# Kernel tuning notes

Hardware: AMD Instinct MI355X
Metric: run time of the kernel (lower is better)

The kernel has to match this reference:

```python
import jax, jax.numpy as jnp
import numpy as np

WS, OWS, NH = 16, 24, 2          # window size, overlap window size (=int(16*0.5)+16), num heads
PAD = (OWS - WS) // 2            # unfold padding = 4


def conv2d(x, w, b):
    kh, kw = w.shape[2], w.shape[3]
    out = jax.lax.conv_general_dilated(x, w, (1, 1), [(kh // 2, kh // 2), (kw // 2, kw // 2)],
                                       dimension_numbers=('NCHW', 'OIHW', 'NCHW'))
    return out + b[None, :, None, None]


def layer_norm(x, g, b, eps=1e-5):
    m = x.mean(-1, keepdims=True)
    v = ((x - m) ** 2).mean(-1, keepdims=True)
    return (x - m) * jax.lax.rsqrt(v + eps) * g + b


def stem(depth, cw1, cb1, cw2, cb2, cw3, cb3, cw4, cb4, in_g, in_b):
    # BasicConv(1->8,k3,relu) -> (8->16,k1,relu) -> (16->16,k3,relu) -> (16->32,k1) -> InstanceNorm2d(32,affine)
    y = jax.nn.relu(conv2d(depth, cw1, cb1))
    y = jax.nn.relu(conv2d(y, cw2, cb2))
    y = jax.nn.relu(conv2d(y, cw3, cb3))
    y = conv2d(y, cw4, cb4)
    m = y.mean((2, 3), keepdims=True)
    v = ((y - m) ** 2).mean((2, 3), keepdims=True)
    return (y - m) * jax.lax.rsqrt(v + 1e-5) * in_g[None, :, None, None] + in_b[None, :, None, None]


def ocab(xq, ykv, rpi, n1g, n1b, wq, bq, wkv, bkv, rpb, wp, bp, n2g, n2b, mw1, mb1, mw2, mb2):
    # Overlapping cross-attention block (HAT-style OCAB, cross variant: q from xq, kv from ykv).
    b, c, h, w = xq.shape
    x = xq.transpose(0, 2, 3, 1)   # b h w c
    y = ykv.transpose(0, 2, 3, 1)
    shortcut = x
    q = layer_norm(x, n1g, n1b) @ wq + bq          # b h w c
    kv = layer_norm(y, n1g, n1b) @ wkv + bkv       # b h w 2c
    nhw, nww = h // WS, w // WS
    # non-overlapping query windows: (b*nw, WS*WS, c)
    qw = q.reshape(b, nhw, WS, nww, WS, c).transpose(0, 1, 3, 2, 4, 5).reshape(b * nhw * nww, WS * WS, c)
    # overlapping kv windows via unfold (patch channel order = (channel, kh, kw), same as torch unfold)
    patches = jax.lax.conv_general_dilated_patches(kv.transpose(0, 3, 1, 2), (OWS, OWS), (WS, WS),
                                                   [(PAD, PAD), (PAD, PAD)])  # b, 2c*OWS*OWS, nhw, nww
    patches = patches.reshape(b, 2, c, OWS * OWS, nhw * nww).transpose(1, 0, 4, 3, 2).reshape(2, b * nhw * nww, OWS * OWS, c)
    k, v = patches[0], patches[1]
    d = c // NH
    qh = qw.reshape(-1, WS * WS, NH, d).transpose(0, 2, 1, 3) * (d ** -0.5)
    kh = k.reshape(-1, OWS * OWS, NH, d).transpose(0, 2, 1, 3)
    vh = v.reshape(-1, OWS * OWS, NH, d).transpose(0, 2, 1, 3)
    attn = jnp.einsum('whqd,whkd->whqk', qh, kh)
    attn = attn + rpb[rpi].transpose(2, 0, 1)[None]  # rel-pos bias -> [1, NH, WS*WS, OWS*OWS]
    attn = jax.nn.softmax(attn, axis=-1)
    out = jnp.einsum('whqk,whkd->whqd', attn, vh).transpose(0, 2, 1, 3).reshape(-1, WS * WS, c)
    # window reverse
    out = out.reshape(b, nhw, nww, WS, WS, c).transpose(0, 1, 3, 2, 4, 5).reshape(b, h, w, c)
    out = out @ wp + bp + shortcut
    out = out + (jax.nn.gelu(layer_norm(out, n2g, n2b) @ mw1 + mb1) @ mw2 + mb2)  # mlp_ratio=2
    return out.transpose(0, 3, 1, 2)


def setup_inputs():
    key = jax.random.key(0)
    ks = jax.random.split(key, 16)
    B, C, H, W = 1, 32, 256, 256
    s = 0.05
    return dict(
        x=jax.random.normal(ks[0], (B, C, H, W), jnp.float32),
        depth=jax.random.normal(ks[1], (B, 1, H, W), jnp.float32),
        rpi=jax.random.randint(ks[2], (WS * WS, OWS * OWS), 0, (WS + OWS - 1) ** 2),
        cw1=jax.random.normal(ks[3], (8, 1, 3, 3)) * s, cb1=jnp.zeros(8),
        cw2=jax.random.normal(ks[4], (16, 8, 1, 1)) * s, cb2=jnp.zeros(16),
        cw3=jax.random.normal(ks[5], (16, 16, 3, 3)) * s, cb3=jnp.zeros(16),
        cw4=jax.random.normal(ks[6], (32, 16, 1, 1)) * s, cb4=jnp.zeros(32),
        in_g=jnp.ones(32), in_b=jnp.zeros(32),
        n1g=jnp.ones(C), n1b=jnp.zeros(C),
        wq=jax.random.normal(ks[7], (C, C)) * s, bq=jnp.zeros(C),
        wkv=jax.random.normal(ks[8], (C, 2 * C)) * s, bkv=jnp.zeros(2 * C),
        rpb=jax.random.normal(ks[9], ((WS + OWS - 1) ** 2, NH)) * 0.02,
        wp=jax.random.normal(ks[10], (C, C)) * s, bp=jnp.zeros(C),
        n2g=jnp.ones(C), n2b=jnp.zeros(C),
        mw1=jax.random.normal(ks[11], (C, 2 * C)) * s, mb1=jnp.zeros(2 * C),
        mw2=jax.random.normal(ks[12], (2 * C, C)) * s, mb2=jnp.zeros(C),
    )


def reference(x, depth, rpi, cw1, cb1, cw2, cb2, cw3, cb3, cw4, cb4, in_g, in_b,
              n1g, n1b, wq, bq, wkv, bkv, rpb, wp, bp, n2g, n2b, mw1, mb1, mw2, mb2):
    f = stem(depth, cw1, cb1, cw2, cb2, cw3, cb3, cw4, cb4, in_g, in_b)
    a = (n1g, n1b, wq, bq, wkv, bkv, rpb, wp, bp, n2g, n2b, mw1, mb1, mw2, mb2)
    out1 = ocab(x, f, rpi, *a)   # shared OCAB weights, called twice with swapped roles
    out2 = ocab(f, x, rpi, *a)
    return out1 + out2 + x
```

## Files before the change

kernel.cpp:

```cpp
#include <hip/hip_runtime.h>
#include <hip/hip_bf16.h>

#define HW 65536
#define KPAD 584

typedef __attribute__((ext_vector_type(8))) short bf8;
typedef __attribute__((ext_vector_type(4))) float f4;

__device__ __forceinline__ unsigned short f2b(float x) {
  unsigned int u = __float_as_uint(x);
  unsigned int r = (u + 0x7fff + ((u >> 16) & 1)) >> 16;
  return (unsigned short)r;
}
__device__ __forceinline__ unsigned int pk2(float lo, float hi) {
  return (__float_as_uint(hi) & 0xffff0000u) | (__float_as_uint(lo) >> 16);
}
__device__ __forceinline__ unsigned int pkrne(float lo, float hi) {
  return ((unsigned int)f2b(hi) << 16) | (unsigned int)f2b(lo);
}
__device__ __forceinline__ float blo(unsigned int u) { return __uint_as_float(u << 16); }
__device__ __forceinline__ float bhi(unsigned int u) { return __uint_as_float(u & 0xffff0000u); }
__device__ __forceinline__ float ex2(float x) { return __builtin_amdgcn_exp2f(x); }

__device__ __forceinline__ void stem_front_body(
    int bx, int t, const float* __restrict__ depth,
    const float* __restrict__ cw1, const float* __restrict__ cb1,
    const float* __restrict__ cw2, const float* __restrict__ cb2,
    float* __restrict__ t2) {
  int p = bx * 256 + t;
  int y = p >> 8, x = p & 255;
  float in9[9];
#pragma unroll
  for (int ky = 0; ky < 3; ky++)
#pragma unroll
    for (int kx = 0; kx < 3; kx++) {
      int yy = y + ky - 1, xx = x + kx - 1;
      bool ok = ((unsigned)yy < 256u) && ((unsigned)xx < 256u);
      in9[ky*3+kx] = ok ? depth[yy*256+xx] : 0.f;
    }
  float t1[8];
#pragma unroll
  for (int o = 0; o < 8; o++) {
    float s = cb1[o];
#pragma unroll
    for (int i = 0; i < 9; i++) s += in9[i] * cw1[o*9+i];
    t1[o] = fmaxf(s, 0.f);
  }
#pragma unroll
  for (int o = 0; o < 16; o++) {
    float s = cb2[o];
#pragma unroll
    for (int ci = 0; ci < 8; ci++) s += t1[ci] * cw2[o*8+ci];
    t2[o*HW + p] = fmaxf(s, 0.f);
  }
}

__device__ __forceinline__ void bias_body(
    int bx, int t, const int* __restrict__ rpi,
    const float* __restrict__ rpb, float* __restrict__ biasT) {
  int idx = bx*256 + t;
  int hd = idx / 147456;
  int rem = idx - hd*147456;
  int qt = rem / 9216;
  int r2 = rem - qt*9216;
  int kb = r2 >> 6;
  int q16 = (r2 >> 2) & 15;
  int r = r2 & 3;
  int key = kb*4 + r;
  int qq = qt*16 + q16;
  biasT[idx] = (rpb[rpi[qq*576 + key]*2 + hd] - 8.0f) * 1.44269504f;
}

__device__ __forceinline__ void lnmm48_body(
    int role, int bx, int t,
    unsigned int* ws16, float* gs, float* bs, float* b2s, float* as_, float* bbs_,
    const float* __restrict__ x, const float* __restrict__ t4,
    const float* __restrict__ part,
    const float* __restrict__ ig, const float* __restrict__ ib,
    const float* __restrict__ n1g, const float* __restrict__ n1b,
    const float* __restrict__ wq, const float* __restrict__ bq,
    const float* __restrict__ wkv, const float* __restrict__ bkv,
    unsigned int* __restrict__ q1, unsigned int* __restrict__ kv1,
    unsigned int* __restrict__ q2, unsigned int* __restrict__ kv2) {
  const float QS = 0.360673503f;
  bool ain = role >= 2;
  int slice = role & 1;
  const float* src = ain ? t4 : x;
  unsigned int* dq  = ain ? q2 : q1;
  unsigned int* dkv = ain ? kv1 : kv2;
  for (int i = t; i < 768; i += 256) {
    int c = i / 24, jw = i - c*24;
    int j = jw*2;
    float a, b;
    if (slice) { a = wkv[c*64 + 16 + j]; b = wkv[c*64 + 16 + j + 1]; }
    else if (j < 32) { a = wq[c*32 + j]; b = wq[c*32 + j + 1]; }
    else { a = wkv[c*64 + (j - 32)]; b = wkv[c*64 + (j - 31)]; }
    ws16[i] = pkrne(a, b);
  }
  if (t < 48) b2s[t] = slice ? bkv[16 + t] : (t < 32 ? bq[t] : bkv[t - 32]);
  if (t < 32) {
    gs[t] = n1g[t]; bs[t] = n1b[t];
    if (ain) {
      float s = 0.f, ss = 0.f;
#pragma unroll
      for (int k = 0; k < 16; k++) { s += part[t*16+k]; ss += part[512 + t*16+k]; }
      float m = s * (1.f/65536.f);
      float var = ss * (1.f/65536.f) - m*m;
      float a = rsqrtf(var + 1e-5f) * ig[t];
      as_[t] = a; bbs_[t] = ib[t] - m*a;
    }
  }
  __syncthreads();
  int p = bx*256 + t;
  float v[32]; float s = 0.f;
  if (ain) {
#pragma unroll
    for (int c = 0; c < 32; c++) { v[c] = src[c*HW+p]*as_[c] + bbs_[c]; s += v[c]; }
  } else {
#pragma unroll
    for (int c = 0; c < 32; c++) { v[c] = src[c*HW+p]; s += v[c]; }
  }
  float m = s * 0.03125f;
  float ss = 0.f;
#pragma unroll
  for (int c = 0; c < 32; c++) { float d = v[c]-m; ss += d*d; }
  float rs = rsqrtf(ss*0.03125f + 1e-5f);
  float acc[48];
#pragma unroll
  for (int j = 0; j < 48; j++) acc[j] = b2s[j];
#pragma unroll
  for (int c = 0; c < 32; c++) {
    float ln = (v[c]-m)*rs*gs[c] + bs[c];
    const uint4* w4 = (const uint4*)&ws16[c*24];
#pragma unroll
    for (int q4 = 0; q4 < 6; q4++) {
      uint4 w = w4[q4];
      acc[q4*8+0] += ln*blo(w.x); acc[q4*8+1] += ln*bhi(w.x);
      acc[q4*8+2] += ln*blo(w.y); acc[q4*8+3] += ln*bhi(w.y);
      acc[q4*8+4] += ln*blo(w.z); acc[q4*8+5] += ln*bhi(w.z);
      acc[q4*8+6] += ln*blo(w.w); acc[q4*8+7] += ln*bhi(w.w);
    }
  }
  if (slice == 0) {
#pragma unroll
    for (int j2 = 0; j2 < 16; j2++)
      dq[j2*HW+p] = pkrne(acc[2*j2]*QS, acc[2*j2+1]*QS);
#pragma unroll
    for (int c2 = 0; c2 < 8; c2++)
      dkv[c2*HW+p] = pkrne(acc[32+2*c2], acc[32+2*c2+1]);
  } else {
#pragma unroll
    for (int c2 = 0; c2 < 24; c2++)
      dkv[(8+c2)*HW+p] = pkrne(acc[2*c2], acc[2*c2+1]);
  }
}

__global__ __launch_bounds__(256) void k_misc(
    const float* __restrict__ depth,
    const float* __restrict__ cw1, const float* __restrict__ cb1,
    const float* __restrict__ cw2, const float* __restrict__ cb2,
    float* __restrict__ t2,
    const int* __restrict__ rpi, const float* __restrict__ rpb, float* __restrict__ biasT,
    const float* __restrict__ x, const float* __restrict__ t4,
    const float* __restrict__ part,
    const float* __restrict__ ig, const float* __restrict__ ib,
    const float* __restrict__ n1g, const float* __restrict__ n1b,
    const float* __restrict__ wq, const float* __restrict__ bq,
    const float* __restrict__ wkv, const float* __restrict__ bkv,
    unsigned int* q1, unsigned int* kv1, unsigned int* q2, unsigned int* kv2) {
  __shared__ __align__(16) unsigned int ws16[768];
  __shared__ float gs[32], bs[32], b2s[48], as_[32], bbs_[32];
  int id = blockIdx.x, t = threadIdx.x;
  if (id < 256) { stem_front_body(id, t, depth, cw1, cb1, cw2, cb2, t2); return; }
  if (id < 1408) { bias_body(id - 256, t, rpi, rpb, biasT); return; }
  int r = id - 1408;
  lnmm48_body(r >> 8, r & 255, t, ws16, gs, bs, b2s, as_, bbs_,
              x, t4, part, ig, ib, n1g, n1b, wq, bq, wkv, bkv, q1, kv1, q2, kv2);
}

__global__ __launch_bounds__(256) void k_lnmmB(
    const float* __restrict__ x, const float* __restrict__ t4,
    const float* __restrict__ part,
    const float* __restrict__ ig, const float* __restrict__ ib,
    const float* __restrict__ n1g, const float* __restrict__ n1b,
    const float* __restrict__ wq, const float* __restrict__ bq,
    const float* __restrict__ wkv, const float* __restrict__ bkv,
    unsigned int* q1, unsigned int* kv1, unsigned int* q2, unsigned int* kv2) {
  __shared__ __align__(16) unsigned int ws16[768];
  __shared__ float gs[32], bs[32], b2s[48], as_[32], bbs_[32];
  lnmm48_body(2 + blockIdx.y, blockIdx.x, threadIdx.x, ws16, gs, bs, b2s, as_, bbs_,
              x, t4, part, ig, ib, n1g, n1b, wq, bq, wkv, bkv, q1, kv1, q2, kv2);
}

__global__ __launch_bounds__(256) void k_conv3(
    const float* __restrict__ t2, const float* __restrict__ cw3,
    const float* __restrict__ cb3, float* __restrict__ t3) {
  int t = threadIdx.x;
  int p = blockIdx.x*256 + t;
  int og = blockIdx.y;
  int y = p >> 8, x = p & 255;
  float acc[4];
#pragma unroll
  for (int o = 0; o < 4; o++) acc[o] = cb3[og*4+o];
#pragma unroll 1
  for (int tap = 0; tap < 9; tap++) {
    int ky = tap/3 - 1, kx = tap - (tap/3)*3 - 1;
    int yy = y+ky, xx = x+kx;
    bool ok = ((unsigned)yy < 256u) && ((unsigned)xx < 256u);
    int pp = yy*256+xx;
#pragma unroll
    for (int ci = 0; ci < 16; ci++) {
      float v = ok ? t2[ci*HW+pp] : 0.f;
#pragma unroll
      for (int o = 0; o < 4; o++)
        acc[o] += v * cw3[(og*4+o)*144 + ci*9 + tap];
    }
  }
#pragma unroll
  for (int o = 0; o < 4; o++) t3[(og*4+o)*HW+p] = fmaxf(acc[o], 0.f);
}

__global__ __launch_bounds__(256) void k_conv4(
    const float* __restrict__ t3, const float* __restrict__ cw4,
    const float* __restrict__ cb4, float* __restrict__ t4) {
  int t = threadIdx.x;
  int p = blockIdx.x*256 + t;
  int og = blockIdx.y;
  float v[16];
#pragma unroll
  for (int ci = 0; ci < 16; ci++) v[ci] = t3[ci*HW+p];
#pragma unroll
  for (int o = 0; o < 8; o++) {
    int oo = og*8 + o;
    float s = cb4[oo];
#pragma unroll
    for (int ci = 0; ci < 16; ci++) s += v[ci]*cw4[oo*16+ci];
    t4[oo*HW+p] = s;
  }
}

__global__ __launch_bounds__(256) void k_instats1(const float* __restrict__ t4,
                                                  float* __restrict__ part) {
  int c = blockIdx.x >> 4, seg = blockIdx.x & 15;
  const float4* src = (const float4*)(t4 + c*HW + seg*4096);
  float s = 0.f, ss = 0.f;
  for (int i = threadIdx.x; i < 1024; i += 256) {
    float4 v = src[i];
    s  += v.x + v.y + v.z + v.w;
    ss += v.x*v.x + v.y*v.y + v.z*v.z + v.w*v.w;
  }
#pragma unroll
  for (int off = 32; off > 0; off >>= 1) {
    s  += __shfl_down(s, off, 64);
    ss += __shfl_down(ss, off, 64);
  }
  __shared__ float sh[8];
  int wid = threadIdx.x >> 6;
  if ((threadIdx.x & 63) == 0) { sh[wid] = s; sh[4+wid] = ss; }
  __syncthreads();
  if (threadIdx.x == 0) {
    part[blockIdx.x]       = sh[0]+sh[1]+sh[2]+sh[3];
    part[512 + blockIdx.x] = sh[4]+sh[5]+sh[6]+sh[7];
  }
}

__global__ __launch_bounds__(256, 4) void k_attn(
    const unsigned int* __restrict__ qA, const unsigned int* __restrict__ kvA,
    float* __restrict__ aoA,
    const unsigned int* __restrict__ qB, const unsigned int* __restrict__ kvB,
    float* __restrict__ aoB,
    const float* __restrict__ biasT) {
  __shared__ __align__(16) unsigned short Ks[576*16];
  __shared__ __align__(16) unsigned short Vt[16*KPAD];

  const unsigned int* q  = blockIdx.y ? qB  : qA;
  const unsigned int* kv = blockIdx.y ? kvB : kvA;
  float* ao              = blockIdx.y ? aoB : aoA;

  int id = blockIdx.x;
  int lin = ((id & 7) << 6) | (id >> 3);
  int wi = lin >> 1, hd = lin & 1;
  int wy = wi >> 4, wx = wi & 15;
  int t = threadIdx.x;
  int by = wy*16 - 4, bx = wx*16 - 4;
  int krow = hd*8, vrow = 16 + hd*8;

  int wave = t >> 6, lane = t & 63;
  int quad = lane >> 4, l16 = lane & 15;
  const bf8 zero8 = {0,0,0,0,0,0,0,0};

  bf8 qf[4];
#pragma unroll
  for (int qi = 0; qi < 4; qi++) {
    if (quad < 2) {
      int qt = wave*4 + qi;
      int prow = (wy*16 + qt)*256 + wx*16 + l16;
      union { unsigned int u[4]; bf8 v; } Q;
#pragma unroll
      for (int jw = 0; jw < 4; jw++)
        Q.u[jw] = q[(krow + quad*4 + jw)*HW + prow];
      qf[qi] = Q.v;
    } else {
      qf[qi] = zero8;
    }
  }

  for (int e = t; e < 576; e += 256) {
    int dy = e / 24, dx = e - dy*24;
    int yy = by + dy, xx = bx + dx;
    bool ok = ((unsigned)yy < 256u) && ((unsigned)xx < 256u);
    int pp = yy*256 + xx;
    int off = e & 31;
    int ppos = ((off & 12) << 1) + ((off >> 4) << 2) + (off & 3);
    int vcol = (e & ~31) + ppos;
    unsigned int kwd[8];
#pragma unroll
    for (int i = 0; i < 8; i++) kwd[i] = ok ? kv[(krow + i)*HW + pp] : 0u;
    *(uint4*)&Ks[e*16]     = *(const uint4*)&kwd[0];
    *(uint4*)&Ks[e*16 + 8] = *(const uint4*)&kwd[4];
#pragma unroll
    for (int i = 0; i < 8; i++) {
      unsigned int vw = ok ? kv[(vrow + i)*HW + pp] : 0u;
      Vt[(2*i)*KPAD + vcol]   = (unsigned short)vw;
      Vt[(2*i+1)*KPAD + vcol] = (unsigned short)(vw >> 16);
    }
  }
  __syncthreads();

  f4 oacc[4];
  float lr[4];
  const float* bb[4];
#pragma unroll
  for (int qi = 0; qi < 4; qi++) {
    int qt = wave*4 + qi;
    oacc[qi] = (f4){0.f,0.f,0.f,0.f};
    lr[qi] = 0.f;
    bb[qi] = biasT + (hd*16 + qt)*9216 + quad*64 + l16*4;
  }

#pragma unroll 2
  for (int kt2 = 0; kt2 < 18; kt2++) {
    int k0 = kt2 * 32;
    bf8 kf0 = zero8, kf1 = zero8;
    if (quad < 2) {
      kf0 = *(const bf8*)&Ks[(k0 + l16)*16 + quad*8];
      kf1 = *(const bf8*)&Ks[(k0 + 16 + l16)*16 + quad*8];
    }
    bf8 vf = *(const bf8*)&Vt[l16*KPAD + k0 + quad*8];
    __builtin_amdgcn_s_setprio(1);
#pragma unroll
    for (int qi = 0; qi < 4; qi++) {
      f4 b0 = *(const f4*)&bb[qi][k0*16];
      f4 b1 = *(const f4*)&bb[qi][(k0+16)*16];
      f4 s0 = __builtin_amdgcn_mfma_f32_16x16x32_bf16(kf0, qf[qi], b0, 0, 0, 0);
      f4 s1 = __builtin_amdgcn_mfma_f32_16x16x32_bf16(kf1, qf[qi], b1, 0, 0, 0);
      float p0[4], p1[4];
#pragma unroll
      for (int r = 0; r < 4; r++) {
        p0[r] = ex2(s0[r]);
        p1[r] = ex2(s1[r]);
        lr[qi] += p0[r] + p1[r];
      }
      union { unsigned int u[4]; bf8 v; } P;
      P.u[0] = pk2(p0[0], p0[1]); P.u[1] = pk2(p0[2], p0[3]);
      P.u[2] = pk2(p1[0], p1[1]); P.u[3] = pk2(p1[2], p1[3]);
      oacc[qi] = __builtin_amdgcn_mfma_f32_16x16x32_bf16(P.v, vf, oacc[qi], 0, 0, 0);
    }
    __builtin_amdgcn_s_setprio(0);
  }
#pragma unroll
  for (int qi = 0; qi < 4; qi++) {
    lr[qi] += __shfl_xor(lr[qi], 16, 64);
    lr[qi] += __shfl_xor(lr[qi], 32, 64);
  }
#pragma unroll
  for (int qi = 0; qi < 4; qi++) {
    int qt = wave*4 + qi;
#pragma unroll
    for (int r = 0; r < 4; r++) {
      float lv = __shfl(lr[qi], quad*4 + r, 64);
      int qw = qt*16 + quad*4 + r;
      ao[(hd*16 + l16)*HW + (wy*16 + (qw >> 4))*256 + wx*16 + (qw & 15)] = oacc[qi][r] / lv;
    }
  }
}

__global__ __launch_bounds__(256) void k_projmlp(
    const float* __restrict__ ao1, const float* __restrict__ ao2,
    const float* __restrict__ x, const float* __restrict__ t4,
    const float* __restrict__ part,
    const float* __restrict__ ig, const float* __restrict__ ib,
    const float* __restrict__ wp, const float* __restrict__ bp,
    const float* __restrict__ n2g, const float* __restrict__ n2b,
    const float* __restrict__ mw1, const float* __restrict__ mb1,
    const float* __restrict__ mw2, const float* __restrict__ mb2,
    float* __restrict__ out) {
  __shared__ __align__(16) float wps[1024];
  __shared__ __align__(16) float w1s[2048];
  __shared__ __align__(16) float w2s[2048];
  __shared__ float bps[32], b1s[64], b2s[32], gs[32], bs[32], as_[32], bbs_[32];
  int t = threadIdx.x;
  for (int i = t; i < 1024; i += 256) wps[i] = wp[i];
  for (int i = t; i < 2048; i += 256) { w1s[i] = mw1[i]; w2s[i] = mw2[i]; }
  if (t < 64) b1s[t] = mb1[t];
  if (t < 32) {
    bps[t] = bp[t]; b2s[t] = mb2[t]; gs[t] = n2g[t]; bs[t] = n2b[t];
    float s = 0.f, ss = 0.f;
#pragma unroll
    for (int k = 0; k < 16; k++) { s += part[t*16+k]; ss += part[512 + t*16+k]; }
    float m = s * (1.f/65536.f);
    float var = ss * (1.f/65536.f) - m*m;
    float a = rsqrtf(var + 1e-5f) * ig[t];
    as_[t] = a; bbs_[t] = ib[t] - m*a;
  }
  __syncthreads();
  int p  = blockIdx.x*128 + (t >> 1);
  int sg = t & 1;
  int jb = sg*16;

  float A[16], B[16];
#pragma unroll
  for (int jj = 0; jj < 16; jj++) { A[jj] = bps[jb+jj]; B[jj] = A[jj]; }
#pragma unroll
  for (int c = 0; c < 32; c++) {
    float va = ao1[c*HW+p];
    float vb = ao2[c*HW+p];
    const float4* w4 = (const float4*)&wps[c*32 + jb];
#pragma unroll
    for (int j4 = 0; j4 < 4; j4++) {
      float4 w = w4[j4];
      A[j4*4+0] += va*w.x; A[j4*4+1] += va*w.y; A[j4*4+2] += va*w.z; A[j4*4+3] += va*w.w;
      B[j4*4+0] += vb*w.x; B[j4*4+1] += vb*w.y; B[j4*4+2] += vb*w.z; B[j4*4+3] += vb*w.w;
    }
  }
  float OUT[16];
#pragma unroll
  for (int jj = 0; jj < 16; jj++) {
    float xv = x[(jb+jj)*HW+p];
    float tv = t4[(jb+jj)*HW+p]*as_[jb+jj] + bbs_[jb+jj];
    A[jj] += xv; B[jj] += tv;
    OUT[jj] = A[jj] + B[jj] + xv + 2.f*b2s[jb+jj];
  }
  float sA = 0.f, sB = 0.f;
#pragma unroll
  for (int jj = 0; jj < 16; jj++) { sA += A[jj]; sB += B[jj]; }
  sA += __shfl_xor(sA, 1, 64);
  sB += __shfl_xor(sB, 1, 64);
  float mA = sA * 0.03125f, mB = sB * 0.03125f;
  float ssA = 0.f, ssB = 0.f;
#pragma unroll
  for (int jj = 0; jj < 16; jj++) {
    float dA = A[jj]-mA, dB = B[jj]-mB;
    ssA += dA*dA; ssB += dB*dB;
  }
  ssA += __shfl_xor(ssA, 1, 64);
  ssB += __shfl_xor(ssB, 1, 64);
  float rsA = rsqrtf(ssA*0.03125f + 1e-5f);
  float rsB = rsqrtf(ssB*0.03125f + 1e-5f);
  float lnA_lo[16], lnA_hi[16], lnB_lo[16], lnB_hi[16];
#pragma unroll
  for (int jj = 0; jj < 16; jj++) {
    float ownA = (A[jj]-mA)*rsA*gs[jb+jj] + bs[jb+jj];
    float ownB = (B[jj]-mB)*rsB*gs[jb+jj] + bs[jb+jj];
    float othA = __shfl_xor(ownA, 1, 64);
    float othB = __shfl_xor(ownB, 1, 64);
    lnA_lo[jj] = sg ? othA : ownA;
    lnA_hi[jj] = sg ? ownA : othA;
    lnB_lo[jj] = sg ? othB : ownB;
    lnB_hi[jj] = sg ? ownB : othB;
  }
  float h0[32], h1[32];
#pragma unroll
  for (int kk = 0; kk < 32; kk++) { h0[kk] = b1s[sg*32+kk]; h1[kk] = h0[kk]; }
#pragma unroll
  for (int c = 0; c < 32; c++) {
    float l0 = (c < 16) ? lnA_lo[c] : lnA_hi[c-16];
    float l1 = (c < 16) ? lnB_lo[c] : lnB_hi[c-16];
    const float4* w4 = (const float4*)&w1s[c*64 + sg*32];
#pragma unroll
    for (int k4 = 0; k4 < 8; k4++) {
      float4 w = w4[k4];
      h0[k4*4+0] += l0*w.x; h0[k4*4+1] += l0*w.y; h0[k4*4+2] += l0*w.z; h0[k4*4+3] += l0*w.w;
      h1[k4*4+0] += l1*w.x; h1[k4*4+1] += l1*w.y; h1[k4*4+2] += l1*w.z; h1[k4*4+3] += l1*w.w;
    }
  }
#pragma unroll
  for (int kk = 0; kk < 32; kk++) {
    float x0 = h0[kk], x1 = h1[kk];
    float u0 = 0.7978845608f * (x0 + 0.044715f*x0*x0*x0);
    float u1 = 0.7978845608f * (x1 + 0.044715f*x1*x1*x1);
    float th0 = 1.f - 2.f/(1.f + __expf(2.f*u0));
    float th1 = 1.f - 2.f/(1.f + __expf(2.f*u1));
    h0[kk] = 0.5f*x0*(1.f + th0) + 0.5f*x1*(1.f + th1);
  }
  float plo[16], phi[16];
#pragma unroll
  for (int jj = 0; jj < 16; jj++) { plo[jj] = 0.f; phi[jj] = 0.f; }
#pragma unroll
  for (int kk = 0; kk < 32; kk++) {
    float gk = h0[kk];
    const float4* w4 = (const float4*)&w2s[(sg*32+kk)*32];
#pragma unroll
    for (int j4 = 0; j4 < 4; j4++) {
      float4 w = w4[j4];
      plo[j4*4+0] += gk*w.x; plo[j4*4+1] += gk*w.y;
      plo[j4*4+2] += gk*w.z; plo[j4*4+3] += gk*w.w;
    }
#pragma unroll
    for (int j4 = 0; j4 < 4; j4++) {
      float4 w = w4[4+j4];
      phi[j4*4+0] += gk*w.x; phi[j4*4+1] += gk*w.y;
      phi[j4*4+2] += gk*w.z; phi[j4*4+3] += gk*w.w;
    }
  }
#pragma unroll
  for (int jj = 0; jj < 16; jj++) {
    float send = sg ? plo[jj] : phi[jj];
    float recv = __shfl_xor(send, 1, 64);
    float own  = sg ? phi[jj] : plo[jj];
    out[(jb+jj)*HW + p] = OUT[jj] + own + recv;
  }
}

extern "C" void kernel_launch(void* const* d_in, const int* in_sizes, int n_in,
                              void* d_out, int out_size, void* d_ws, size_t ws_size,
                              hipStream_t stream) {
  const float* x    = (const float*)d_in[0];
  const float* depth= (const float*)d_in[1];
  const int*   rpi  = (const int*)d_in[2];
  const float* cw1  = (const float*)d_in[3],  *cb1 = (const float*)d_in[4];
  const float* cw2  = (const float*)d_in[5],  *cb2 = (const float*)d_in[6];
  const float* cw3  = (const float*)d_in[7],  *cb3 = (const float*)d_in[8];
  const float* cw4  = (const float*)d_in[9],  *cb4 = (const float*)d_in[10];
  const float* in_g = (const float*)d_in[11], *in_b = (const float*)d_in[12];
  const float* n1g  = (const float*)d_in[13], *n1b = (const float*)d_in[14];
  const float* wq   = (const float*)d_in[15], *bq  = (const float*)d_in[16];
  const float* wkv  = (const float*)d_in[17], *bkv = (const float*)d_in[18];
  const float* rpb  = (const float*)d_in[19];
  const float* wp   = (const float*)d_in[20], *bp  = (const float*)d_in[21];
  const float* n2g  = (const float*)d_in[22], *n2b = (const float*)d_in[23];
  const float* mw1  = (const float*)d_in[24], *mb1 = (const float*)d_in[25];
  const float* mw2  = (const float*)d_in[26], *mb2 = (const float*)d_in[27];

  float* W   = (float*)d_ws;
  float* o1  = (float*)d_out;

  float* t4    = W;
  unsigned int* q1  = (unsigned int*)(W + 2097152);
  unsigned int* q2  = (unsigned int*)(W + 3145728);
  unsigned int* kv1 = (unsigned int*)(W + 4194304);
  unsigned int* kv2 = (unsigned int*)(W + 6291456);
  float* ao1   = W + 8388608;
  float* ao2   = W + 10485760;
  float* biasT = W + 12582912;
  float* part  = W + 12877824;
  float* t2 = ao1;
  float* t3 = ao2;

  k_misc   <<<1920, 256, 0, stream>>>(depth, cw1, cb1, cw2, cb2, t2,
                                      rpi, rpb, biasT,
                                      x, t4, part, in_g, in_b, n1g, n1b,
                                      wq, bq, wkv, bkv, q1, kv1, q2, kv2);
  k_conv3  <<<dim3(256,4), 256, 0, stream>>>(t2, cw3, cb3, t3);
  k_conv4  <<<dim3(256,4), 256, 0, stream>>>(t3, cw4, cb4, t4);
  k_instats1<<<512, 256, 0, stream>>>(t4, part);
  k_lnmmB  <<<dim3(256,2), 256, 0, stream>>>(x, t4, part, in_g, in_b, n1g, n1b,
                                             wq, bq, wkv, bkv, q1, kv1, q2, kv2);
  k_attn   <<<dim3(512,2), 256, 0, stream>>>(q1, kv1, ao1, q2, kv2, ao2, biasT);
  k_projmlp<<<512, 256, 0, stream>>>(ao1, ao2, x, t4, part, in_g, in_b,
                                     wp, bp, n2g, n2b, mw1, mb1, mw2, mb2, o1);
}
```

Measured before the change: 238.9 us.

## Pack attention bias as bf16 pairs, fuse instance stats into conv4, MFMA row sums

Stores the relative position bias as packed bf16 pairs instead of fp32, which halves bias memory traffic in the attention loop and shrinks the bias-building part of k_misc. Instance-norm statistics are now reduced inside k_conv4 with wave shuffles and atomics, removing the separate k_instats1 launch and its reread of t4. Softmax row sums are computed with an extra MFMA against a ones vector instead of scalar adds and cross-lane shuffles. The risks are reduced bias precision, the constant -8 offset being dropped from the bias, and single-pass float atomics for the variance, which can lose precision.

```diff
diff --git a/kernel.cpp b/kernel.cpp
--- a/kernel.cpp
+++ b/kernel.cpp
@@ -55,20 +55,22 @@
   }
 }
 
-__device__ __forceinline__ void bias_body(
+__device__ __forceinline__ void bias_pk_body(
     int bx, int t, const int* __restrict__ rpi,
-    const float* __restrict__ rpb, float* __restrict__ biasT) {
+    const float* __restrict__ rpb, unsigned int* __restrict__ biasPk) {
   int idx = bx*256 + t;
-  int hd = idx / 147456;
-  int rem = idx - hd*147456;
-  int qt = rem / 9216;
-  int r2 = rem - qt*9216;
-  int kb = r2 >> 6;
-  int q16 = (r2 >> 2) & 15;
-  int r = r2 & 3;
-  int key = kb*4 + r;
-  int qq = qt*16 + q16;
-  biasT[idx] = (rpb[rpi[qq*576 + key]*2 + hd] - 8.0f) * 1.44269504f;
+  int hd = idx / 36864;
+  int rem = idx - hd*36864;
+  int qt = rem / 4608;
+  int r2 = rem - qt*4608;
+  int kt2 = r2 >> 8;
+  int w8 = r2 & 255;
+  int quad = w8 >> 6, q = (w8 >> 2) & 15, r = w8 & 3;
+  int klo = kt2*32 + quad*4 + r;
+  int qq = qt*16 + q;
+  float lo = rpb[rpi[qq*576 + klo]*2 + hd] * 1.44269504f;
+  float hi = rpb[rpi[qq*576 + klo + 16]*2 + hd] * 1.44269504f;
+  biasPk[idx] = pkrne(lo, hi);
 }
 
 __device__ __forceinline__ void lnmm48_body(
@@ -101,11 +103,8 @@
   if (t < 32) {
     gs[t] = n1g[t]; bs[t] = n1b[t];
     if (ain) {
-      float s = 0.f, ss = 0.f;
-#pragma unroll
-      for (int k = 0; k < 16; k++) { s += part[t*16+k]; ss += part[512 + t*16+k]; }
-      float m = s * (1.f/65536.f);
-      float var = ss * (1.f/65536.f) - m*m;
+      float m = part[t] * (1.f/65536.f);
+      float var = part[32+t] * (1.f/65536.f) - m*m;
       float a = rsqrtf(var + 1e-5f) * ig[t];
       as_[t] = a; bbs_[t] = ib[t] - m*a;
     }
@@ -160,9 +159,9 @@
     const float* __restrict__ cw1, const float* __restrict__ cb1,
     const float* __restrict__ cw2, const float* __restrict__ cb2,
     float* __restrict__ t2,
-    const int* __restrict__ rpi, const float* __restrict__ rpb, float* __restrict__ biasT,
+    const int* __restrict__ rpi, const float* __restrict__ rpb,
+    unsigned int* __restrict__ biasPk, float* __restrict__ part,
     const float* __restrict__ x, const float* __restrict__ t4,
-    const float* __restrict__ part,
     const float* __restrict__ ig, const float* __restrict__ ib,
     const float* __restrict__ n1g, const float* __restrict__ n1b,
     const float* __restrict__ wq, const float* __restrict__ bq,
@@ -172,8 +171,12 @@
   __shared__ float gs[32], bs[32], b2s[48], as_[32], bbs_[32];
   int id = blockIdx.x, t = threadIdx.x;
   if (id < 256) { stem_front_body(id, t, depth, cw1, cb1, cw2, cb2, t2); return; }
-  if (id < 1408) { bias_body(id - 256, t, rpi, rpb, biasT); return; }
-  int r = id - 1408;
+  if (id < 544) {
+    if (id == 256 && t < 64) part[t] = 0.f;
+    bias_pk_body(id - 256, t, rpi, rpb, biasPk);
+    return;
+  }
+  int r = id - 544;
   lnmm48_body(r >> 8, r & 255, t, ws16, gs, bs, b2s, as_, bbs_,
               x, t4, part, ig, ib, n1g, n1b, wq, bq, wkv, bkv, q1, kv1, q2, kv2);
 }
@@ -222,13 +225,15 @@
 
 __global__ __launch_bounds__(256) void k_conv4(
     const float* __restrict__ t3, const float* __restrict__ cw4,
-    const float* __restrict__ cb4, float* __restrict__ t4) {
+    const float* __restrict__ cb4, float* __restrict__ t4,
+    float* __restrict__ part) {
   int t = threadIdx.x;
   int p = blockIdx.x*256 + t;
   int og = blockIdx.y;
   float v[16];
 #pragma unroll
   for (int ci = 0; ci < 16; ci++) v[ci] = t3[ci*HW+p];
+  float s8[8], q8[8];
 #pragma unroll
   for (int o = 0; o < 8; o++) {
     int oo = og*8 + o;
@@ -236,31 +241,27 @@
 #pragma unroll
     for (int ci = 0; ci < 16; ci++) s += v[ci]*cw4[oo*16+ci];
     t4[oo*HW+p] = s;
-  }
-}
-
-__global__ __launch_bounds__(256) void k_instats1(const float* __restrict__ t4,
-                                                  float* __restrict__ part) {
-  int c = blockIdx.x >> 4, seg = blockIdx.x & 15;
-  const float4* src = (const float4*)(t4 + c*HW + seg*4096);
-  float s = 0.f, ss = 0.f;
-  for (int i = threadIdx.x; i < 1024; i += 256) {
-    float4 v = src[i];
-    s  += v.x + v.y + v.z + v.w;
-    ss += v.x*v.x + v.y*v.y + v.z*v.z + v.w*v.w;
-  }
-#pragma unroll
-  for (int off = 32; off > 0; off >>= 1) {
-    s  += __shfl_down(s, off, 64);
-    ss += __shfl_down(ss, off, 64);
-  }
-  __shared__ float sh[8];
-  int wid = threadIdx.x >> 6;
-  if ((threadIdx.x & 63) == 0) { sh[wid] = s; sh[4+wid] = ss; }
+    s8[o] = s; q8[o] = s*s;
+  }
+#pragma unroll
+  for (int off = 1; off < 64; off <<= 1) {
+#pragma unroll
+    for (int o = 0; o < 8; o++) {
+      s8[o] += __shfl_xor(s8[o], off, 64);
+      q8[o] += __shfl_xor(q8[o], off, 64);
+    }
+  }
+  __shared__ float red[4][16];
+  int wid = t >> 6, lane = t & 63;
+  if (lane == 0) {
+#pragma unroll
+    for (int o = 0; o < 8; o++) { red[wid][o] = s8[o]; red[wid][8+o] = q8[o]; }
+  }
   __syncthreads();
-  if (threadIdx.x == 0) {
-    part[blockIdx.x]       = sh[0]+sh[1]+sh[2]+sh[3];
-    part[512 + blockIdx.x] = sh[4]+sh[5]+sh[6]+sh[7];
+  if (t < 16) {
+    float acc = red[0][t] + red[1][t] + red[2][t] + red[3][t];
+    int o = t & 7;
+    atomicAdd(&part[(t < 8 ? 0 : 32) + og*8 + o], acc);
   }
 }
 
@@ -269,7 +270,7 @@
     float* __restrict__ aoA,
     const unsigned int* __restrict__ qB, const unsigned int* __restrict__ kvB,
     float* __restrict__ aoB,
-    const float* __restrict__ biasT) {
+    const unsigned int* __restrict__ biasPk) {
   __shared__ __align__(16) unsigned short Ks[576*16];
   __shared__ __align__(16) unsigned short Vt[16*KPAD];
 
@@ -288,6 +289,7 @@
   int wave = t >> 6, lane = t & 63;
   int quad = lane >> 4, l16 = lane & 15;
   const bf8 zero8 = {0,0,0,0,0,0,0,0};
+  const bf8 ones8 = {0x3F80,0x3F80,0x3F80,0x3F80,0x3F80,0x3F80,0x3F80,0x3F80};
 
   bf8 qf[4];
 #pragma unroll
@@ -328,15 +330,13 @@
   __syncthreads();
 
   f4 oacc[4];
-  float lr[4];
-  const float* bb[4];
+  f4 lacc[4];
 #pragma unroll
   for (int qi = 0; qi < 4; qi++) {
-    int qt = wave*4 + qi;
     oacc[qi] = (f4){0.f,0.f,0.f,0.f};
-    lr[qi] = 0.f;
-    bb[qi] = biasT + (hd*16 + qt)*9216 + quad*64 + l16*4;
-  }
+    lacc[qi] = (f4){0.f,0.f,0.f,0.f};
+  }
+  unsigned int bb0 = (unsigned)((hd*8 + wave*4)*4608 + quad*64 + l16*4);
 
 #pragma unroll 2
   for (int kt2 = 0; kt2 < 18; kt2++) {
@@ -350,8 +350,12 @@
     __builtin_amdgcn_s_setprio(1);
 #pragma unroll
     for (int qi = 0; qi < 4; qi++) {
-      f4 b0 = *(const f4*)&bb[qi][k0*16];
-      f4 b1 = *(const f4*)&bb[qi][(k0+16)*16];
+      uint4 bw = *(const uint4*)&biasPk[bb0 + qi*4608 + kt2*256];
+      f4 b0, b1;
+      b0[0] = blo(bw.x); b1[0] = bhi(bw.x);
+      b0[1] = blo(bw.y); b1[1] = bhi(bw.y);
+      b0[2] = blo(bw.z); b1[2] = bhi(bw.z);
+      b0[3] = blo(bw.w); b1[3] = bhi(bw.w);
       f4 s0 = __builtin_amdgcn_mfma_f32_16x16x32_bf16(kf0, qf[qi], b0, 0, 0, 0);
       f4 s1 = __builtin_amdgcn_mfma_f32_16x16x32_bf16(kf1, qf[qi], b1, 0, 0, 0);
       float p0[4], p1[4];
@@ -359,28 +363,23 @@
       for (int r = 0; r < 4; r++) {
         p0[r] = ex2(s0[r]);
         p1[r] = ex2(s1[r]);
-        lr[qi] += p0[r] + p1[r];
       }
       union { unsigned int u[4]; bf8 v; } P;
       P.u[0] = pk2(p0[0], p0[1]); P.u[1] = pk2(p0[2], p0[3]);
       P.u[2] = pk2(p1[0], p1[1]); P.u[3] = pk2(p1[2], p1[3]);
       oacc[qi] = __builtin_amdgcn_mfma_f32_16x16x32_bf16(P.v, vf, oacc[qi], 0, 0, 0);
+      lacc[qi] = __builtin_amdgcn_mfma_f32_16x16x32_bf16(P.v, ones8, lacc[qi], 0, 0, 0);
     }
     __builtin_amdgcn_s_setprio(0);
-  }
-#pragma unroll
-  for (int qi = 0; qi < 4; qi++) {
-    lr[qi] += __shfl_xor(lr[qi], 16, 64);
-    lr[qi] += __shfl_xor(lr[qi], 32, 64);
   }
 #pragma unroll
   for (int qi = 0; qi < 4; qi++) {
     int qt = wave*4 + qi;
 #pragma unroll
     for (int r = 0; r < 4; r++) {
-      float lv = __shfl(lr[qi], quad*4 + r, 64);
       int qw = qt*16 + quad*4 + r;
-      ao[(hd*16 + l16)*HW + (wy*16 + (qw >> 4))*256 + wx*16 + (qw & 15)] = oacc[qi][r] / lv;
+      ao[(hd*16 + l16)*HW + (wy*16 + (qw >> 4))*256 + wx*16 + (qw & 15)] =
+          oacc[qi][r] / lacc[qi][r];
     }
   }
 }
@@ -405,11 +404,8 @@
   if (t < 64) b1s[t] = mb1[t];
   if (t < 32) {
     bps[t] = bp[t]; b2s[t] = mb2[t]; gs[t] = n2g[t]; bs[t] = n2b[t];
-    float s = 0.f, ss = 0.f;
-#pragma unroll
-    for (int k = 0; k < 16; k++) { s += part[t*16+k]; ss += part[512 + t*16+k]; }
-    float m = s * (1.f/65536.f);
-    float var = ss * (1.f/65536.f) - m*m;
+    float m = part[t] * (1.f/65536.f);
+    float var = part[32+t] * (1.f/65536.f) - m*m;
     float a = rsqrtf(var + 1e-5f) * ig[t];
     as_[t] = a; bbs_[t] = ib[t] - m*a;
   }
@@ -552,21 +548,20 @@
   unsigned int* kv2 = (unsigned int*)(W + 6291456);
   float* ao1   = W + 8388608;
   float* ao2   = W + 10485760;
-  float* biasT = W + 12582912;
+  unsigned int* biasPk = (unsigned int*)(W + 12582912);
   float* part  = W + 12877824;
   float* t2 = ao1;
   float* t3 = ao2;
 
-  k_misc   <<<1920, 256, 0, stream>>>(depth, cw1, cb1, cw2, cb2, t2,
-                                      rpi, rpb, biasT,
-                                      x, t4, part, in_g, in_b, n1g, n1b,
+  k_misc   <<<1056, 256, 0, stream>>>(depth, cw1, cb1, cw2, cb2, t2,
+                                      rpi, rpb, biasPk, part,
+                                      x, t4, in_g, in_b, n1g, n1b,
                                       wq, bq, wkv, bkv, q1, kv1, q2, kv2);
   k_conv3  <<<dim3(256,4), 256, 0, stream>>>(t2, cw3, cb3, t3);
-  k_conv4  <<<dim3(256,4), 256, 0, stream>>>(t3, cw4, cb4, t4);
-  k_instats1<<<512, 256, 0, stream>>>(t4, part);
+  k_conv4  <<<dim3(256,4), 256, 0, stream>>>(t3, cw4, cb4, t4, part);
   k_lnmmB  <<<dim3(256,2), 256, 0, stream>>>(x, t4, part, in_g, in_b, n1g, n1b,
                                              wq, bq, wkv, bkv, q1, kv1, q2, kv2);
-  k_attn   <<<dim3(512,2), 256, 0, stream>>>(q1, kv1, ao1, q2, kv2, ao2, biasT);
+  k_attn   <<<dim3(512,2), 256, 0, stream>>>(q1, kv1, ao1, q2, kv2, ao2, biasPk);
   k_projmlp<<<512, 256, 0, stream>>>(ao1, ao2, x, t4, part, in_g, in_b,
                                      wp, bp, n2g, n2b, mw1, mb1, mw2, mb2, o1);
 }
```

Result: slower. 349.0 us (+46.1%).

## Pack attention bias to bf16 pairs and compute row sums via MFMA

Applied to the files above, without the earlier changes.

The relative-position bias table is stored as packed bf16 pairs, with the two key halves in one word. This halves the bias bytes the attention kernel reads per tile and shrinks the bias-generation launch. The softmax denominator is now accumulated by an extra MFMA of the probability tile against a ones matrix, replacing per-lane scalar sums and the cross-lane shuffles. The constant -8 offset on the bias is dropped and bias precision drops to bf16, which risks exp2 overflow or accuracy differences.

```diff
diff --git a/kernel.cpp b/kernel.cpp
--- a/kernel.cpp
+++ b/kernel.cpp
@@ -55,20 +55,22 @@
   }
 }
 
-__device__ __forceinline__ void bias_body(
+__device__ __forceinline__ void bias_pk_body(
     int bx, int t, const int* __restrict__ rpi,
-    const float* __restrict__ rpb, float* __restrict__ biasT) {
+    const float* __restrict__ rpb, unsigned int* __restrict__ biasPk) {
   int idx = bx*256 + t;
-  int hd = idx / 147456;
-  int rem = idx - hd*147456;
-  int qt = rem / 9216;
-  int r2 = rem - qt*9216;
-  int kb = r2 >> 6;
-  int q16 = (r2 >> 2) & 15;
-  int r = r2 & 3;
-  int key = kb*4 + r;
+  int hd = idx / 73728;
+  int rem = idx - hd*73728;
+  int qt = rem / 4608;
+  int r2 = rem - qt*4608;
+  int kt2 = r2 >> 8;
+  int w8 = r2 & 255;
+  int quad = w8 >> 6, q16 = (w8 >> 2) & 15, r = w8 & 3;
+  int klo = kt2*32 + quad*4 + r;
   int qq = qt*16 + q16;
-  biasT[idx] = (rpb[rpi[qq*576 + key]*2 + hd] - 8.0f) * 1.44269504f;
+  float lo = rpb[rpi[qq*576 + klo]*2 + hd] * 1.44269504f;
+  float hi = rpb[rpi[qq*576 + klo + 16]*2 + hd] * 1.44269504f;
+  biasPk[idx] = pkrne(lo, hi);
 }
 
 __device__ __forceinline__ void lnmm48_body(
@@ -160,7 +162,8 @@
     const float* __restrict__ cw1, const float* __restrict__ cb1,
     const float* __restrict__ cw2, const float* __restrict__ cb2,
     float* __restrict__ t2,
-    const int* __restrict__ rpi, const float* __restrict__ rpb, float* __restrict__ biasT,
+    const int* __restrict__ rpi, const float* __restrict__ rpb,
+    unsigned int* __restrict__ biasPk,
     const float* __restrict__ x, const float* __restrict__ t4,
     const float* __restrict__ part,
     const float* __restrict__ ig, const float* __restrict__ ib,
@@ -172,8 +175,8 @@
   __shared__ float gs[32], bs[32], b2s[48], as_[32], bbs_[32];
   int id = blockIdx.x, t = threadIdx.x;
   if (id < 256) { stem_front_body(id, t, depth, cw1, cb1, cw2, cb2, t2); return; }
-  if (id < 1408) { bias_body(id - 256, t, rpi, rpb, biasT); return; }
-  int r = id - 1408;
+  if (id < 832) { bias_pk_body(id - 256, t, rpi, rpb, biasPk); return; }
+  int r = id - 832;
   lnmm48_body(r >> 8, r & 255, t, ws16, gs, bs, b2s, as_, bbs_,
               x, t4, part, ig, ib, n1g, n1b, wq, bq, wkv, bkv, q1, kv1, q2, kv2);
 }
@@ -269,7 +272,7 @@
     float* __restrict__ aoA,
     const unsigned int* __restrict__ qB, const unsigned int* __restrict__ kvB,
     float* __restrict__ aoB,
-    const float* __restrict__ biasT) {
+    const unsigned int* __restrict__ biasPk) {
   __shared__ __align__(16) unsigned short Ks[576*16];
   __shared__ __align__(16) unsigned short Vt[16*KPAD];
 
@@ -288,6 +291,7 @@
   int wave = t >> 6, lane = t & 63;
   int quad = lane >> 4, l16 = lane & 15;
   const bf8 zero8 = {0,0,0,0,0,0,0,0};
+  const bf8 ones8 = {0x3F80,0x3F80,0x3F80,0x3F80,0x3F80,0x3F80,0x3F80,0x3F80};
 
   bf8 qf[4];
 #pragma unroll
@@ -328,15 +332,13 @@
   __syncthreads();
 
   f4 oacc[4];
-  float lr[4];
-  const float* bb[4];
+  f4 lacc[4];
 #pragma unroll
   for (int qi = 0; qi < 4; qi++) {
-    int qt = wave*4 + qi;
     oacc[qi] = (f4){0.f,0.f,0.f,0.f};
-    lr[qi] = 0.f;
-    bb[qi] = biasT + (hd*16 + qt)*9216 + quad*64 + l16*4;
-  }
+    lacc[qi] = (f4){0.f,0.f,0.f,0.f};
+  }
+  unsigned int bb0 = (unsigned)((hd*16 + wave*4)*4608 + quad*64 + l16*4);
 
 #pragma unroll 2
   for (int kt2 = 0; kt2 < 18; kt2++) {
@@ -350,8 +352,12 @@
     __builtin_amdgcn_s_setprio(1);
 #pragma unroll
     for (int qi = 0; qi < 4; qi++) {
-      f4 b0 = *(const f4*)&bb[qi][k0*16];
-      f4 b1 = *(const f4*)&bb[qi][(k0+16)*16];
+      uint4 bw = *(const uint4*)&biasPk[bb0 + qi*4608 + kt2*256];
+      f4 b0, b1;
+      b0[0] = blo(bw.x); b1[0] = bhi(bw.x);
+      b0[1] = blo(bw.y); b1[1] = bhi(bw.y);
+      b0[2] = blo(bw.z); b1[2] = bhi(bw.z);
+      b0[3] = blo(bw.w); b1[3] = bhi(bw.w);
       f4 s0 = __builtin_amdgcn_mfma_f32_16x16x32_bf16(kf0, qf[qi], b0, 0, 0, 0);
       f4 s1 = __builtin_amdgcn_mfma_f32_16x16x32_bf16(kf1, qf[qi], b1, 0, 0, 0);
       float p0[4], p1[4];
@@ -359,28 +365,23 @@
       for (int r = 0; r < 4; r++) {
         p0[r] = ex2(s0[r]);
         p1[r] = ex2(s1[r]);
-        lr[qi] += p0[r] + p1[r];
       }
       union { unsigned int u[4]; bf8 v; } P;
       P.u[0] = pk2(p0[0], p0[1]); P.u[1] = pk2(p0[2], p0[3]);
       P.u[2] = pk2(p1[0], p1[1]); P.u[3] = pk2(p1[2], p1[3]);
       oacc[qi] = __builtin_amdgcn_mfma_f32_16x16x32_bf16(P.v, vf, oacc[qi], 0, 0, 0);
+      lacc[qi] = __builtin_amdgcn_mfma_f32_16x16x32_bf16(P.v, ones8, lacc[qi], 0, 0, 0);
     }
     __builtin_amdgcn_s_setprio(0);
-  }
-#pragma unroll
-  for (int qi = 0; qi < 4; qi++) {
-    lr[qi] += __shfl_xor(lr[qi], 16, 64);
-    lr[qi] += __shfl_xor(lr[qi], 32, 64);
   }
 #pragma unroll
   for (int qi = 0; qi < 4; qi++) {
     int qt = wave*4 + qi;
 #pragma unroll
     for (int r = 0; r < 4; r++) {
-      float lv = __shfl(lr[qi], quad*4 + r, 64);
       int qw = qt*16 + quad*4 + r;
-      ao[(hd*16 + l16)*HW + (wy*16 + (qw >> 4))*256 + wx*16 + (qw & 15)] = oacc[qi][r] / lv;
+      ao[(hd*16 + l16)*HW + (wy*16 + (qw >> 4))*256 + wx*16 + (qw & 15)] =
+          oacc[qi][r] / lacc[qi][r];
     }
   }
 }
@@ -552,13 +553,13 @@
   unsigned int* kv2 = (unsigned int*)(W + 6291456);
   float* ao1   = W + 8388608;
   float* ao2   = W + 10485760;
-  float* biasT = W + 12582912;
+  unsigned int* biasPk = (unsigned int*)(W + 12582912);
   float* part  = W + 12877824;
   float* t2 = ao1;
   float* t3 = ao2;
 
-  k_misc   <<<1920, 256, 0, stream>>>(depth, cw1, cb1, cw2, cb2, t2,
-                                      rpi, rpb, biasT,
+  k_misc   <<<1344, 256, 0, stream>>>(depth, cw1, cb1, cw2, cb2, t2,
+                                      rpi, rpb, biasPk,
                                       x, t4, part, in_g, in_b, n1g, n1b,
                                       wq, bq, wkv, bkv, q1, kv1, q2, kv2);
   k_conv3  <<<dim3(256,4), 256, 0, stream>>>(t2, cw3, cb3, t3);
@@ -566,7 +567,7 @@
   k_instats1<<<512, 256, 0, stream>>>(t4, part);
   k_lnmmB  <<<dim3(256,2), 256, 0, stream>>>(x, t4, part, in_g, in_b, n1g, n1b,
                                              wq, bq, wkv, bkv, q1, kv1, q2, kv2);
-  k_attn   <<<dim3(512,2), 256, 0, stream>>>(q1, kv1, ao1, q2, kv2, ao2, biasT);
+  k_attn   <<<dim3(512,2), 256, 0, stream>>>(q1, kv1, ao1, q2, kv2, ao2, biasPk);
   k_projmlp<<<512, 256, 0, stream>>>(ao1, ao2, x, t4, part, in_g, in_b,
                                      wp, bp, n2g, n2b, mw1, mb1, mw2, mb2, o1);
 }
```

Measured after the change: 238.6 us, median of 2. Within noise of the previous version (-0.1%).
